# Kernel tuning notes

Hardware: AMD Instinct MI355X
Metric: run time of the kernel (lower is better)

## Reference

```python
import jax, jax.numpy as jnp
import numpy as np

B, S, H, DH = 2, 4096, 8, 64
D = H * DH  # 512

def setup_inputs() -> dict:
    key = jax.random.key(0)
    ks = jax.random.split(key, 9)
    sc = 1.0 / np.sqrt(D)
    return {
        "hidden_states": jax.random.normal(ks[0], (B, S, D), jnp.float32),
        "Wq": jax.random.normal(ks[1], (D, D), jnp.float32) * sc,
        "bq": jax.random.normal(ks[2], (D,), jnp.float32) * 0.02,
        "Wk": jax.random.normal(ks[3], (D, D), jnp.float32) * sc,
        "bk": jax.random.normal(ks[4], (D,), jnp.float32) * 0.02,
        "Wv": jax.random.normal(ks[5], (D, D), jnp.float32) * sc,
        "bv": jax.random.normal(ks[6], (D,), jnp.float32) * 0.02,
        "Wo": jax.random.normal(ks[7], (D, D), jnp.float32) * sc,
        "bo": jax.random.normal(ks[8], (D,), jnp.float32) * 0.02,
    }

def _split_heads(t):
    # (B, S, H*DH) -> (B, H, S, DH)
    b = t.shape[0]
    return t.reshape(b, S, H, DH).transpose(0, 2, 1, 3)

def reference(hidden_states, Wq, bq, Wk, bk, Wv, bv, Wo, bo):
    q = _split_heads(hidden_states @ Wq + bq)
    k = _split_heads(hidden_states @ Wk + bk)
    v = _split_heads(hidden_states @ Wv + bv)
    scale = 1.0 / jnp.sqrt(jnp.asarray(DH, q.dtype))
    energy = jnp.einsum('bhqd,bhkd->bhqk', q, k) * scale
    weights = jax.nn.softmax(energy, axis=-1)  # full O(S^2) matrix, as in source
    attended = jnp.einsum('bhqv,bhvd->bhqd', weights, v)
    merged = attended.transpose(0, 2, 1, 3).reshape(hidden_states.shape[0], S, D)
    return merged @ Wo + bo
```

## Files before the change

### kernel.cpp

```cpp
#include <hip/hip_runtime.h>
#include <cstdint>

typedef __bf16 bf16;
typedef __bf16 bf16x4 __attribute__((ext_vector_type(4)));
typedef __bf16 bf16x8 __attribute__((ext_vector_type(8)));
typedef float floatx4 __attribute__((ext_vector_type(4)));

#define MFMA32(a, b, c) __builtin_amdgcn_mfma_f32_16x16x32_bf16((a), (b), (c), 0, 0, 0)
#define MFMA16(a, b, c) __builtin_amdgcn_mfma_f32_16x16x16bf16_1k((a), (b), (c), 0, 0, 0)

__device__ inline bf16x8 cvt8(const float* p) {
    float4 u = *(const float4*)p;
    float4 v = *(const float4*)(p + 4);
    bf16x8 r;
    r[0] = (bf16)u.x; r[1] = (bf16)u.y; r[2] = (bf16)u.z; r[3] = (bf16)u.w;
    r[4] = (bf16)v.x; r[5] = (bf16)v.y; r[6] = (bf16)v.z; r[7] = (bf16)v.w;
    return r;
}

__global__ __launch_bounds__(256) void k_transpose(
    const float* __restrict__ w0, const float* __restrict__ w1,
    const float* __restrict__ w2, const float* __restrict__ w3,
    bf16* __restrict__ o0, bf16* __restrict__ o1,
    bf16* __restrict__ o2, bf16* __restrict__ o3)
{
    __shared__ float t[32][33];
    const float* in;
    bf16* out;
    switch (blockIdx.z) {
        case 0: in = w0; out = o0; break;
        case 1: in = w1; out = o1; break;
        case 2: in = w2; out = o2; break;
        default: in = w3; out = o3; break;
    }
    const int tx = threadIdx.x & 31;
    const int ty = threadIdx.x >> 5;
    const int r0 = blockIdx.y * 32;
    const int c0 = blockIdx.x * 32;
    #pragma unroll
    for (int i = 0; i < 32; i += 8)
        t[ty + i][tx] = in[(size_t)(r0 + ty + i) * 512 + c0 + tx];
    __syncthreads();
    #pragma unroll
    for (int i = 0; i < 32; i += 8)
        out[(size_t)(c0 + ty + i) * 512 + r0 + tx] = (bf16)t[tx][ty + i];
}

__global__ __launch_bounds__(256) void k_cvtx(
    const float* __restrict__ X, bf16* __restrict__ Xb)
{
    const size_t idx = ((size_t)blockIdx.x * 256 + threadIdx.x) * 8;
    *(bf16x8*)(Xb + idx) = cvt8(X + idx);
}

__global__ __launch_bounds__(256) void k_qkv(
    const bf16* __restrict__ Xb, const bf16* __restrict__ Wcat,
    const float* __restrict__ bq, const float* __restrict__ bk, const float* __restrict__ bv,
    bf16* __restrict__ Qs, bf16* __restrict__ Ks, bf16* __restrict__ Vt)
{
    __shared__ __align__(16) unsigned char smem[36864];
    uint4* Al = (uint4*)smem;
    uint4* Bl = (uint4*)(smem + 16384);

    const int tid  = threadIdx.x;
    const int w    = tid >> 6;
    const int lane = tid & 63;
    const int col  = lane & 15;
    const int quad = lane >> 4;
    const int m0 = blockIdx.x * 128;
    const int n0 = blockIdx.y * 128;

    const bf16* gA0 = Xb   + (size_t)(m0 + (tid >> 2)) * 512 + (tid & 3) * 8;
    const bf16* gA1 = gA0 + 64 * 512;
    const bf16* gB0 = Wcat + (size_t)(n0 + (tid >> 2)) * 512 + (tid & 3) * 8;
    const bf16* gB1 = gB0 + 64 * 512;

    const floatx4 zf = {0.f, 0.f, 0.f, 0.f};
    floatx4 acc[4][4];
    #pragma unroll
    for (int a = 0; a < 4; ++a)
        #pragma unroll
        for (int b = 0; b < 4; ++b) acc[a][b] = zf;

    Al[tid]       = *(const uint4*)gA0;
    Al[tid + 256] = *(const uint4*)gA1;
    Bl[tid]       = *(const uint4*)gB0;
    Bl[tid + 256] = *(const uint4*)gB1;
    __syncthreads();

    const int mb = (w & 1) * 64;
    const int nb = (w >> 1) * 64;

    int buf = 0;
    for (int kk = 0; kk < 16; ++kk) {
        const int kn = ((kk + 1) & 15) * 32;
        const uint4 pa0 = *(const uint4*)(gA0 + kn);
        const uint4 pa1 = *(const uint4*)(gA1 + kn);
        const uint4 pb0 = *(const uint4*)(gB0 + kn);
        const uint4 pb1 = *(const uint4*)(gB1 + kn);

        const uint4* A4 = Al + buf * 512;
        const uint4* B4 = Bl + buf * 512;
        bf16x8 af[4], bfr[4];
        #pragma unroll
        for (int t = 0; t < 4; ++t) {
            union { uint4 u; bf16x8 v; } ca, cb;
            ca.u = A4[(mb + 16 * t + col) * 4 + quad];
            cb.u = B4[(nb + 16 * t + col) * 4 + quad];
            af[t] = ca.v;
            bfr[t] = cb.v;
        }
        #pragma unroll
        for (int tm = 0; tm < 4; ++tm)
            #pragma unroll
            for (int tn = 0; tn < 4; ++tn)
                acc[tm][tn] = MFMA32(af[tm], bfr[tn], acc[tm][tn]);

        const int nbuf = buf ^ 1;
        Al[nbuf * 512 + tid]       = pa0;
        Al[nbuf * 512 + tid + 256] = pa1;
        Bl[nbuf * 512 + tid]       = pb0;
        Bl[nbuf * 512 + tid + 256] = pb1;
        __syncthreads();
        buf = nbuf;
    }

    bf16* ep = (bf16*)smem + (size_t)w * 64 * 72;

    const int which = blockIdx.y >> 2;
    const int nbase = (blockIdx.y & 3) * 128 + nb;
    const int h  = nbase >> 6;
    const int mw = m0 + mb;
    const int b  = mw >> 12;
    const int s0 = mw & 4095;
    const float qsc = 0.125f * 1.44269504088896f;

    if (which == 2) {
        #pragma unroll
        for (int tn = 0; tn < 4; ++tn) {
            const int d = 16 * tn + col;
            const float bb = bv[nbase + d];
            #pragma unroll
            for (int tm = 0; tm < 4; ++tm) {
                union { bf16 e[4]; uint2 u; } pk;
                #pragma unroll
                for (int r = 0; r < 4; ++r) pk.e[r] = (bf16)(acc[tm][tn][r] + bb);
                *(uint2*)(ep + d * 72 + 16 * tm + 4 * quad) = pk.u;
            }
        }
    } else {
        const float* bias = (which == 0) ? bq : bk;
        const float sc = (which == 0) ? qsc : 1.0f;
        #pragma unroll
        for (int tn = 0; tn < 4; ++tn) {
            const int d = 16 * tn + col;
            const float bb = bias[nbase + d];
            #pragma unroll
            for (int tm = 0; tm < 4; ++tm)
                #pragma unroll
                for (int r = 0; r < 4; ++r)
                    ep[(16 * tm + 4 * quad + r) * 72 + d] = (bf16)((acc[tm][tn][r] + bb) * sc);
        }
    }

    asm volatile("" ::: "memory");

    const int rl = lane >> 3;
    const int ch = lane & 7;
    bf16* gbase;
    size_t rowstride;
    if (which == 2) {
        gbase = Vt + (((size_t)b * 8 + h) * 64) * 4096 + s0;
        rowstride = 4096;
    } else {
        bf16* P = (which == 0) ? Qs : Ks;
        gbase = P + (((size_t)b * 8 + h) * 4096 + s0) * 64;
        rowstride = 64;
    }
    #pragma unroll
    for (int it = 0; it < 8; ++it) {
        const int row = it * 8 + rl;
        const uint4 v = *(const uint4*)(ep + row * 72 + ch * 8);
        *(uint4*)(gbase + (size_t)row * rowstride + ch * 8) = v;
    }
}

__global__ __launch_bounds__(256, 2) void k_attn(
    const bf16* __restrict__ Qs, const bf16* __restrict__ Ks, const bf16* __restrict__ Vt,
    bf16* __restrict__ att)
{
    __shared__ uint4 Klds[2][256];
    __shared__ uint4 Vlds[2][256];

    const int tid  = threadIdx.x;
    const int w    = tid >> 6;
    const int lane = tid & 63;
    const int col  = lane & 15;
    const int quad = lane >> 4;
    const int i    = blockIdx.x;
    const int bh   = ((i & 7) << 1) | ((i >> 3) & 1);
    const int q0   = (i >> 4) * 128 + w * 32;

    const bf16* Qb = Qs + (size_t)bh * 262144;
    const bf16* Kb = Ks + (size_t)bh * 262144;
    const bf16* Vb = Vt + (size_t)bh * 262144;

    const int rK  = tid >> 3;
    const int lcK = (tid & 7) ^ (rK & 7);
    const bf16* gK = Kb + (size_t)rK * 64 + lcK * 8;
    const int pV  = tid >> 3;
    const int ccV = (tid & 7) ^ (pV & 7);
    const int dV  = 2 * pV + (ccV >> 2);
    const int cV  = ccV & 3;
    const bf16* gV = Vb + (size_t)dV * 4096 + cV * 8;

    bf16x8 aq[2][2];
    #pragma unroll
    for (int s = 0; s < 2; ++s)
        #pragma unroll
        for (int c = 0; c < 2; ++c)
            aq[s][c] = *(const bf16x8*)(Qb + (size_t)(q0 + 16 * s + col) * 64 + 32 * c + quad * 8);

    const floatx4 zf = {0.f, 0.f, 0.f, 0.f};
    floatx4 o[2][4];
    float lsum[2] = {0.f, 0.f};
    #pragma unroll
    for (int s = 0; s < 2; ++s)
        #pragma unroll
        for (int dt = 0; dt < 4; ++dt) o[s][dt] = zf;

    const int c1 = col & 1, ch = col >> 1, qh = quad >> 1, ql = quad & 1;

    Klds[0][tid] = *(const uint4*)gK;
    Vlds[0][tid] = *(const uint4*)gV;
    __syncthreads();

    int buf = 0;
    for (int kt = 0; kt < 4096; kt += 32) {
        const int kn = (kt + 32) & 4095;
        const uint4 kreg = *(const uint4*)(gK + (size_t)kn * 64);
        const uint4 vreg = *(const uint4*)(gV + kn);

        const uint4* Kl = Klds[buf];
        const uint2* Vl = (const uint2*)Vlds[buf];

        bf16x8 kf[2][2];
        #pragma unroll
        for (int t = 0; t < 2; ++t)
            #pragma unroll
            for (int c = 0; c < 2; ++c) {
                union { uint4 u; bf16x8 v; } cv;
                cv.u = Kl[(16 * t + col) * 8 + ((quad + 4 * c) ^ (col & 7))];
                kf[t][c] = cv.v;
            }
        bf16x4 vfrag[4][2];
        #pragma unroll
        for (int dt = 0; dt < 4; ++dt)
            #pragma unroll
            for (int t = 0; t < 2; ++t) {
                const int slot = (dt * 8 + ch) * 8 + ((c1 * 4 + 2 * t + qh) ^ ch);
                union { uint2 u; bf16x4 v; } cv;
                cv.u = Vl[slot * 2 + ql];
                vfrag[dt][t] = cv.v;
            }

        #pragma unroll
        for (int s = 0; s < 2; ++s) {
            bf16x4 pw[2];
            #pragma unroll
            for (int t = 0; t < 2; ++t) {
                floatx4 sc = MFMA32(kf[t][1], aq[s][1], MFMA32(kf[t][0], aq[s][0], zf));
                const float p0 = __builtin_amdgcn_exp2f(sc[0]);
                const float p1 = __builtin_amdgcn_exp2f(sc[1]);
                const float p2 = __builtin_amdgcn_exp2f(sc[2]);
                const float p3 = __builtin_amdgcn_exp2f(sc[3]);
                lsum[s] += (p0 + p1) + (p2 + p3);
                union { bf16 e[4]; bf16x4 v; } pk;
                pk.e[0] = (bf16)p0; pk.e[1] = (bf16)p1;
                pk.e[2] = (bf16)p2; pk.e[3] = (bf16)p3;
                pw[t] = pk.v;
            }
            #pragma unroll
            for (int dt = 0; dt < 4; ++dt) {
                o[s][dt] = MFMA16(vfrag[dt][0], pw[0], o[s][dt]);
                o[s][dt] = MFMA16(vfrag[dt][1], pw[1], o[s][dt]);
            }
        }

        Klds[buf ^ 1][tid] = kreg;
        Vlds[buf ^ 1][tid] = vreg;
        __syncthreads();
        buf ^= 1;
    }

    float inv[2];
    #pragma unroll
    for (int s = 0; s < 2; ++s) {
        float v = lsum[s];
        v += __shfl_xor(v, 16, 64);
        v += __shfl_xor(v, 32, 64);
        inv[s] = 1.0f / v;
    }

    const int b = bh >> 3;
    const int h = bh & 7;
    #pragma unroll
    for (int s = 0; s < 2; ++s)
        #pragma unroll
        for (int dt = 0; dt < 4; ++dt) {
            union { bf16 e[4]; uint2 u; } pk;
            #pragma unroll
            for (int r = 0; r < 4; ++r) pk.e[r] = (bf16)(o[s][dt][r] * inv[s]);
            const size_t row = (size_t)b * 4096 + q0 + 16 * s + col;
            *(uint2*)(att + row * 512 + h * 64 + 16 * dt + 4 * quad) = pk.u;
        }
}

__global__ __launch_bounds__(256) void k_oproj(
    const bf16* __restrict__ att, const bf16* __restrict__ Wto,
    const float* __restrict__ bo, float* __restrict__ out)
{
    __shared__ uint4 Al[2][512];
    __shared__ uint4 Bl[2][512];

    const int tid  = threadIdx.x;
    const int w    = tid >> 6;
    const int lane = tid & 63;
    const int col  = lane & 15;
    const int quad = lane >> 4;
    const int m0 = blockIdx.x * 128;
    const int n0 = blockIdx.y * 128;

    const bf16* gA0 = att + (size_t)(m0 + (tid >> 2)) * 512 + (tid & 3) * 8;
    const bf16* gA1 = gA0 + 64 * 512;
    const bf16* gB0 = Wto + (size_t)(n0 + (tid >> 2)) * 512 + (tid & 3) * 8;
    const bf16* gB1 = gB0 + 64 * 512;

    const floatx4 zf = {0.f, 0.f, 0.f, 0.f};
    floatx4 acc[4][4];
    #pragma unroll
    for (int a = 0; a < 4; ++a)
        #pragma unroll
        for (int b = 0; b < 4; ++b) acc[a][b] = zf;

    Al[0][tid]       = *(const uint4*)gA0;
    Al[0][tid + 256] = *(const uint4*)gA1;
    Bl[0][tid]       = *(const uint4*)gB0;
    Bl[0][tid + 256] = *(const uint4*)gB1;
    __syncthreads();

    const int mb = (w & 1) * 64;
    const int nb = (w >> 1) * 64;

    int buf = 0;
    for (int kk = 0; kk < 16; ++kk) {
        const int kn = ((kk + 1) & 15) * 32;
        const uint4 pa0 = *(const uint4*)(gA0 + kn);
        const uint4 pa1 = *(const uint4*)(gA1 + kn);
        const uint4 pb0 = *(const uint4*)(gB0 + kn);
        const uint4 pb1 = *(const uint4*)(gB1 + kn);

        const uint4* A4 = Al[buf];
        const uint4* B4 = Bl[buf];
        bf16x8 af[4], bfr[4];
        #pragma unroll
        for (int t = 0; t < 4; ++t) {
            union { uint4 u; bf16x8 v; } ca, cb;
            ca.u = A4[(mb + 16 * t + col) * 4 + quad];
            cb.u = B4[(nb + 16 * t + col) * 4 + quad];
            af[t] = ca.v;
            bfr[t] = cb.v;
        }
        #pragma unroll
        for (int tm = 0; tm < 4; ++tm)
            #pragma unroll
            for (int tn = 0; tn < 4; ++tn)
                acc[tm][tn] = MFMA32(af[tm], bfr[tn], acc[tm][tn]);

        Al[buf ^ 1][tid]       = pa0;
        Al[buf ^ 1][tid + 256] = pa1;
        Bl[buf ^ 1][tid]       = pb0;
        Bl[buf ^ 1][tid + 256] = pb1;
        __syncthreads();
        buf ^= 1;
    }

    #pragma unroll
    for (int tn = 0; tn < 4; ++tn) {
        const int n = n0 + nb + 16 * tn + col;
        const float bb = bo[n];
        #pragma unroll
        for (int tm = 0; tm < 4; ++tm)
            #pragma unroll
            for (int r = 0; r < 4; ++r) {
                const int m = m0 + mb + 16 * tm + quad * 4 + r;
                out[(size_t)m * 512 + n] = acc[tm][tn][r] + bb;
            }
    }
}

extern "C" void kernel_launch(void* const* d_in, const int* in_sizes, int n_in,
                              void* d_out, int out_size, void* d_ws, size_t ws_size,
                              hipStream_t stream)
{
    const float* X  = (const float*)d_in[0];
    const float* Wq = (const float*)d_in[1];
    const float* bq = (const float*)d_in[2];
    const float* Wk = (const float*)d_in[3];
    const float* bk = (const float*)d_in[4];
    const float* Wv = (const float*)d_in[5];
    const float* bv = (const float*)d_in[6];
    const float* Wo = (const float*)d_in[7];
    const float* bo = (const float*)d_in[8];

    bf16* Wtq = (bf16*)d_ws;
    bf16* Wtk = Wtq + 512 * 512;
    bf16* Wtv = Wtk + 512 * 512;
    bf16* Wto = Wtv + 512 * 512;
    bf16* Qs  = Wto + 512 * 512;
    bf16* Ks  = Qs + (size_t)16 * 4096 * 64;
    bf16* Vt  = Ks + (size_t)16 * 4096 * 64;
    bf16* att = Vt + (size_t)16 * 4096 * 64;

    bf16* Xb  = (bf16*)d_out;

    k_transpose<<<dim3(16, 16, 4), 256, 0, stream>>>(Wq, Wk, Wv, Wo, Wtq, Wtk, Wtv, Wto);
    k_cvtx<<<2048, 256, 0, stream>>>(X, Xb);
    k_qkv<<<dim3(64, 12), 256, 0, stream>>>(Xb, Wtq, bq, bk, bv, Qs, Ks, Vt);
    k_attn<<<512, 256, 0, stream>>>(Qs, Ks, Vt, att);
    k_oproj<<<dim3(64, 4), 256, 0, stream>>>(att, Wto, bo, (float*)d_out);
}
```

Before: 205.1 us.

## Enlarge attention query tile, switch PV to 16x16x32 MFMA, fuse prep kernels, shrink oproj tile

Each attention wave now handles 64 query rows instead of 32, so every K/V tile loaded into shared memory is reused across twice as many queries and half as many blocks are launched. The V layout in shared memory becomes padded rows (80-byte stride), which lets the PV product use the wider 16x16x32 MFMA with bf16x8 fragments. The qkv epilogue V-transpose store slots are permuted to match that layout. The weight-transpose and X-convert kernels are merged into one launch, and the output projection uses 128x64 tiles to double the block count. The changes risk higher register pressure in attention, the launch_bounds occupancy hint is dropped, and only 256 attention blocks may underfill the GPU.

```diff
diff --git a/kernel.cpp b/kernel.cpp
--- a/kernel.cpp
+++ b/kernel.cpp
@@ -2,12 +2,10 @@
 #include <cstdint>
 
 typedef __bf16 bf16;
-typedef __bf16 bf16x4 __attribute__((ext_vector_type(4)));
 typedef __bf16 bf16x8 __attribute__((ext_vector_type(8)));
 typedef float floatx4 __attribute__((ext_vector_type(4)));
 
 #define MFMA32(a, b, c) __builtin_amdgcn_mfma_f32_16x16x32_bf16((a), (b), (c), 0, 0, 0)
-#define MFMA16(a, b, c) __builtin_amdgcn_mfma_f32_16x16x16bf16_1k((a), (b), (c), 0, 0, 0)
 
 __device__ inline bf16x8 cvt8(const float* p) {
     float4 u = *(const float4*)p;
@@ -18,16 +16,25 @@
     return r;
 }
 
-__global__ __launch_bounds__(256) void k_transpose(
+__global__ __launch_bounds__(256) void k_prep(
     const float* __restrict__ w0, const float* __restrict__ w1,
     const float* __restrict__ w2, const float* __restrict__ w3,
+    const float* __restrict__ X,
     bf16* __restrict__ o0, bf16* __restrict__ o1,
-    bf16* __restrict__ o2, bf16* __restrict__ o3)
+    bf16* __restrict__ o2, bf16* __restrict__ o3,
+    bf16* __restrict__ Xb)
 {
     __shared__ float t[32][33];
+    const int z = blockIdx.z;
+    if (z >= 4) {
+        const int idx = (z - 4) * 256 + blockIdx.y * 16 + blockIdx.x;
+        const size_t e = ((size_t)idx * 256 + threadIdx.x) * 8;
+        *(bf16x8*)(Xb + e) = cvt8(X + e);
+        return;
+    }
     const float* in;
     bf16* out;
-    switch (blockIdx.z) {
+    switch (z) {
         case 0: in = w0; out = o0; break;
         case 1: in = w1; out = o1; break;
         case 2: in = w2; out = o2; break;
@@ -44,13 +51,6 @@
     #pragma unroll
     for (int i = 0; i < 32; i += 8)
         out[(size_t)(c0 + ty + i) * 512 + r0 + tx] = (bf16)t[tx][ty + i];
-}
-
-__global__ __launch_bounds__(256) void k_cvtx(
-    const float* __restrict__ X, bf16* __restrict__ Xb)
-{
-    const size_t idx = ((size_t)blockIdx.x * 256 + threadIdx.x) * 8;
-    *(bf16x8*)(Xb + idx) = cvt8(X + idx);
 }
 
 __global__ __launch_bounds__(256) void k_qkv(
@@ -145,7 +145,8 @@
                 union { bf16 e[4]; uint2 u; } pk;
                 #pragma unroll
                 for (int r = 0; r < 4; ++r) pk.e[r] = (bf16)(acc[tm][tn][r] + bb);
-                *(uint2*)(ep + d * 72 + 16 * tm + 4 * quad) = pk.u;
+                const int sl = 32 * (tm >> 1) + 8 * quad + 4 * (tm & 1);
+                *(uint2*)(ep + d * 72 + sl) = pk.u;
             }
         }
     } else {
@@ -185,12 +186,12 @@
     }
 }
 
-__global__ __launch_bounds__(256, 2) void k_attn(
+__global__ __launch_bounds__(256) void k_attn(
     const bf16* __restrict__ Qs, const bf16* __restrict__ Ks, const bf16* __restrict__ Vt,
     bf16* __restrict__ att)
 {
     __shared__ uint4 Klds[2][256];
-    __shared__ uint4 Vlds[2][256];
+    __shared__ __align__(16) unsigned char Vlds[2][64 * 80];
 
     const int tid  = threadIdx.x;
     const int w    = tid >> 6;
@@ -199,7 +200,7 @@
     const int quad = lane >> 4;
     const int i    = blockIdx.x;
     const int bh   = ((i & 7) << 1) | ((i >> 3) & 1);
-    const int q0   = (i >> 4) * 128 + w * 32;
+    const int q0   = (i >> 4) * 256 + w * 64;
 
     const bf16* Qb = Qs + (size_t)bh * 262144;
     const bf16* Kb = Ks + (size_t)bh * 262144;
@@ -208,31 +209,28 @@
     const int rK  = tid >> 3;
     const int lcK = (tid & 7) ^ (rK & 7);
     const bf16* gK = Kb + (size_t)rK * 64 + lcK * 8;
-    const int pV  = tid >> 3;
-    const int ccV = (tid & 7) ^ (pV & 7);
-    const int dV  = 2 * pV + (ccV >> 2);
-    const int cV  = ccV & 3;
+    const int dV = tid >> 2;
+    const int cV = tid & 3;
     const bf16* gV = Vb + (size_t)dV * 4096 + cV * 8;
-
-    bf16x8 aq[2][2];
-    #pragma unroll
-    for (int s = 0; s < 2; ++s)
+    const int vOff = dV * 80 + cV * 16;
+
+    bf16x8 aq[4][2];
+    #pragma unroll
+    for (int s = 0; s < 4; ++s)
         #pragma unroll
         for (int c = 0; c < 2; ++c)
             aq[s][c] = *(const bf16x8*)(Qb + (size_t)(q0 + 16 * s + col) * 64 + 32 * c + quad * 8);
 
     const floatx4 zf = {0.f, 0.f, 0.f, 0.f};
-    floatx4 o[2][4];
-    float lsum[2] = {0.f, 0.f};
-    #pragma unroll
-    for (int s = 0; s < 2; ++s)
+    floatx4 o[4][4];
+    float lsum[4] = {0.f, 0.f, 0.f, 0.f};
+    #pragma unroll
+    for (int s = 0; s < 4; ++s)
         #pragma unroll
         for (int dt = 0; dt < 4; ++dt) o[s][dt] = zf;
 
-    const int c1 = col & 1, ch = col >> 1, qh = quad >> 1, ql = quad & 1;
-
     Klds[0][tid] = *(const uint4*)gK;
-    Vlds[0][tid] = *(const uint4*)gV;
+    *(uint4*)(Vlds[0] + vOff) = *(const uint4*)gV;
     __syncthreads();
 
     int buf = 0;
@@ -242,7 +240,7 @@
         const uint4 vreg = *(const uint4*)(gV + kn);
 
         const uint4* Kl = Klds[buf];
-        const uint2* Vl = (const uint2*)Vlds[buf];
+        const unsigned char* Vlb = Vlds[buf];
 
         bf16x8 kf[2][2];
         #pragma unroll
@@ -253,20 +251,17 @@
                 cv.u = Kl[(16 * t + col) * 8 + ((quad + 4 * c) ^ (col & 7))];
                 kf[t][c] = cv.v;
             }
-        bf16x4 vfrag[4][2];
-        #pragma unroll
-        for (int dt = 0; dt < 4; ++dt)
-            #pragma unroll
-            for (int t = 0; t < 2; ++t) {
-                const int slot = (dt * 8 + ch) * 8 + ((c1 * 4 + 2 * t + qh) ^ ch);
-                union { uint2 u; bf16x4 v; } cv;
-                cv.u = Vl[slot * 2 + ql];
-                vfrag[dt][t] = cv.v;
-            }
-
-        #pragma unroll
-        for (int s = 0; s < 2; ++s) {
-            bf16x4 pw[2];
+        bf16x8 vf[4];
+        #pragma unroll
+        for (int dt = 0; dt < 4; ++dt) {
+            union { uint4 u; bf16x8 v; } cv;
+            cv.u = *(const uint4*)(Vlb + (16 * dt + col) * 80 + quad * 16);
+            vf[dt] = cv.v;
+        }
+
+        #pragma unroll
+        for (int s = 0; s < 4; ++s) {
+            union { bf16 e[8]; bf16x8 v; } pk;
             #pragma unroll
             for (int t = 0; t < 2; ++t) {
                 floatx4 sc = MFMA32(kf[t][1], aq[s][1], MFMA32(kf[t][0], aq[s][0], zf));
@@ -275,27 +270,25 @@
                 const float p2 = __builtin_amdgcn_exp2f(sc[2]);
                 const float p3 = __builtin_amdgcn_exp2f(sc[3]);
                 lsum[s] += (p0 + p1) + (p2 + p3);
-                union { bf16 e[4]; bf16x4 v; } pk;
-                pk.e[0] = (bf16)p0; pk.e[1] = (bf16)p1;
-                pk.e[2] = (bf16)p2; pk.e[3] = (bf16)p3;
-                pw[t] = pk.v;
+                pk.e[4 * t + 0] = (bf16)p0;
+                pk.e[4 * t + 1] = (bf16)p1;
+                pk.e[4 * t + 2] = (bf16)p2;
+                pk.e[4 * t + 3] = (bf16)p3;
             }
             #pragma unroll
-            for (int dt = 0; dt < 4; ++dt) {
-                o[s][dt] = MFMA16(vfrag[dt][0], pw[0], o[s][dt]);
-                o[s][dt] = MFMA16(vfrag[dt][1], pw[1], o[s][dt]);
-            }
+            for (int dt = 0; dt < 4; ++dt)
+                o[s][dt] = MFMA32(vf[dt], pk.v, o[s][dt]);
         }
 
         Klds[buf ^ 1][tid] = kreg;
-        Vlds[buf ^ 1][tid] = vreg;
+        *(uint4*)(Vlds[buf ^ 1] + vOff) = vreg;
         __syncthreads();
         buf ^= 1;
     }
 
-    float inv[2];
-    #pragma unroll
-    for (int s = 0; s < 2; ++s) {
+    float inv[4];
+    #pragma unroll
+    for (int s = 0; s < 4; ++s) {
         float v = lsum[s];
         v += __shfl_xor(v, 16, 64);
         v += __shfl_xor(v, 32, 64);
@@ -305,7 +298,7 @@
     const int b = bh >> 3;
     const int h = bh & 7;
     #pragma unroll
-    for (int s = 0; s < 2; ++s)
+    for (int s = 0; s < 4; ++s)
         #pragma unroll
         for (int dt = 0; dt < 4; ++dt) {
             union { bf16 e[4]; uint2 u; } pk;
@@ -321,7 +314,7 @@
     const float* __restrict__ bo, float* __restrict__ out)
 {
     __shared__ uint4 Al[2][512];
-    __shared__ uint4 Bl[2][512];
+    __shared__ uint4 Bl[2][256];
 
     const int tid  = threadIdx.x;
     const int w    = tid >> 6;
@@ -329,28 +322,26 @@
     const int col  = lane & 15;
     const int quad = lane >> 4;
     const int m0 = blockIdx.x * 128;
-    const int n0 = blockIdx.y * 128;
+    const int n0 = blockIdx.y * 64;
 
     const bf16* gA0 = att + (size_t)(m0 + (tid >> 2)) * 512 + (tid & 3) * 8;
     const bf16* gA1 = gA0 + 64 * 512;
     const bf16* gB0 = Wto + (size_t)(n0 + (tid >> 2)) * 512 + (tid & 3) * 8;
-    const bf16* gB1 = gB0 + 64 * 512;
 
     const floatx4 zf = {0.f, 0.f, 0.f, 0.f};
-    floatx4 acc[4][4];
+    floatx4 acc[4][2];
     #pragma unroll
     for (int a = 0; a < 4; ++a)
         #pragma unroll
-        for (int b = 0; b < 4; ++b) acc[a][b] = zf;
+        for (int b = 0; b < 2; ++b) acc[a][b] = zf;
 
     Al[0][tid]       = *(const uint4*)gA0;
     Al[0][tid + 256] = *(const uint4*)gA1;
     Bl[0][tid]       = *(const uint4*)gB0;
-    Bl[0][tid + 256] = *(const uint4*)gB1;
     __syncthreads();
 
     const int mb = (w & 1) * 64;
-    const int nb = (w >> 1) * 64;
+    const int nb = (w >> 1) * 32;
 
     int buf = 0;
     for (int kk = 0; kk < 16; ++kk) {
@@ -358,35 +349,37 @@
         const uint4 pa0 = *(const uint4*)(gA0 + kn);
         const uint4 pa1 = *(const uint4*)(gA1 + kn);
         const uint4 pb0 = *(const uint4*)(gB0 + kn);
-        const uint4 pb1 = *(const uint4*)(gB1 + kn);
 
         const uint4* A4 = Al[buf];
         const uint4* B4 = Bl[buf];
-        bf16x8 af[4], bfr[4];
+        bf16x8 af[4], bfr[2];
         #pragma unroll
         for (int t = 0; t < 4; ++t) {
-            union { uint4 u; bf16x8 v; } ca, cb;
+            union { uint4 u; bf16x8 v; } ca;
             ca.u = A4[(mb + 16 * t + col) * 4 + quad];
+            af[t] = ca.v;
+        }
+        #pragma unroll
+        for (int t = 0; t < 2; ++t) {
+            union { uint4 u; bf16x8 v; } cb;
             cb.u = B4[(nb + 16 * t + col) * 4 + quad];
-            af[t] = ca.v;
             bfr[t] = cb.v;
         }
         #pragma unroll
         for (int tm = 0; tm < 4; ++tm)
             #pragma unroll
-            for (int tn = 0; tn < 4; ++tn)
+            for (int tn = 0; tn < 2; ++tn)
                 acc[tm][tn] = MFMA32(af[tm], bfr[tn], acc[tm][tn]);
 
         Al[buf ^ 1][tid]       = pa0;
         Al[buf ^ 1][tid + 256] = pa1;
         Bl[buf ^ 1][tid]       = pb0;
-        Bl[buf ^ 1][tid + 256] = pb1;
         __syncthreads();
         buf ^= 1;
     }
 
     #pragma unroll
-    for (int tn = 0; tn < 4; ++tn) {
+    for (int tn = 0; tn < 2; ++tn) {
         const int n = n0 + nb + 16 * tn + col;
         const float bb = bo[n];
         #pragma unroll
@@ -424,9 +417,9 @@
 
     bf16* Xb  = (bf16*)d_out;
 
-    k_transpose<<<dim3(16, 16, 4), 256, 0, stream>>>(Wq, Wk, Wv, Wo, Wtq, Wtk, Wtv, Wto);
-    k_cvtx<<<2048, 256, 0, stream>>>(X, Xb);
+    k_prep<<<dim3(16, 16, 12), 256, 0, stream>>>(Wq, Wk, Wv, Wo, X,
+                                                 Wtq, Wtk, Wtv, Wto, Xb);
     k_qkv<<<dim3(64, 12), 256, 0, stream>>>(Xb, Wtq, bq, bk, bv, Qs, Ks, Vt);
-    k_attn<<<512, 256, 0, stream>>>(Qs, Ks, Vt, att);
-    k_oproj<<<dim3(64, 4), 256, 0, stream>>>(att, Wto, bo, (float*)d_out);
-}
+    k_attn<<<256, 256, 0, stream>>>(Qs, Ks, Vt, att);
+    k_oproj<<<dim3(64, 8), 256, 0, stream>>>(att, Wto, bo, (float*)d_out);
+}
```

Measured after the change: 228.7 us. 1.12x slower.
